# Kernel tuning notes

Hardware: AMD Instinct MI355X
Metric: run time of the kernel (lower is better)

The kernel has to match this reference:

```python
import jax, jax.numpy as jnp
import numpy as np

B, S, E, H, L, F = 64, 256, 480, 6, 8, 1920
D = E // H  # 80
VOCAB, MEL, CHORD = 4833, 257, 4833 - 257
EPS = 1e-5


def setup_inputs() -> dict:
    key = jax.random.key(0)
    ks = jax.random.split(key, 24)
    mel = jax.random.randint(ks[0], (B, S), 0, MEL)
    chd = MEL + jax.random.randint(ks[1], (B, S), 0, CHORD)
    pos = jnp.arange(S) % 2  # 0=melody, 1=chord
    input_tokens = jnp.where(pos[None, :] == 1, chd, mel)
    std = 0.02
    n = lambda k, shp: std * jax.random.normal(k, shp, dtype=jnp.float32)
    return {
        'input_tokens': input_tokens,
        'tok_emb': n(ks[2], (VOCAB, E)),
        'pos_emb': n(ks[3], (S, E)),
        'Wq': n(ks[4], (L, E, E)), 'bq': jnp.zeros((L, E)),
        'Wk': n(ks[5], (L, E, E)), 'bk': jnp.zeros((L, E)),
        'Wv': n(ks[6], (L, E, E)), 'bv': jnp.zeros((L, E)),
        'Wo': n(ks[7], (L, E, E)), 'bo': jnp.zeros((L, E)),
        'ln1_s': jnp.ones((L, E)), 'ln1_b': jnp.zeros((L, E)),
        'ln2_s': jnp.ones((L, E)), 'ln2_b': jnp.zeros((L, E)),
        'W1': n(ks[8], (L, F, E)), 'b1': jnp.zeros((L, F)),
        'W2': n(ks[9], (L, E, F)), 'b2': jnp.zeros((L, E)),
        'Wh': n(ks[10], (CHORD, E)), 'bh': jnp.zeros((CHORD,)),
    }


def _ln(x, s, b):
    mu = jnp.mean(x, -1, keepdims=True)
    var = jnp.var(x, -1, keepdims=True)
    return (x - mu) * jax.lax.rsqrt(var + EPS) * s + b


def reference(input_tokens, tok_emb, pos_emb, Wq, bq, Wk, bk, Wv, bv, Wo, bo,
              ln1_s, ln1_b, ln2_s, ln2_b, W1, b1, W2, b2, Wh, bh):
    x = tok_emb[input_tokens] + pos_emb[None, :, :]  # [B,S,E]
    causal = jnp.tril(jnp.ones((S, S), dtype=bool))  # True = keep
    scale = 1.0 / jnp.sqrt(jnp.float32(D))
    for i in range(L):
        h = _ln(x, ln1_s[i], ln1_b[i])
        q = (h @ Wq[i].T + bq[i]).reshape(B, S, H, D).transpose(0, 2, 1, 3)
        k = (h @ Wk[i].T + bk[i]).reshape(B, S, H, D).transpose(0, 2, 1, 3)
        v = (h @ Wv[i].T + bv[i]).reshape(B, S, H, D).transpose(0, 2, 1, 3)
        scores = jnp.einsum('bhsd,bhtd->bhst', q, k) * scale
        scores = jnp.where(causal[None, None], scores, -jnp.inf)
        attn = jax.nn.softmax(scores, axis=-1)
        o = jnp.einsum('bhst,bhtd->bhsd', attn, v)
        o = o.transpose(0, 2, 1, 3).reshape(B, S, E)
        x = x + (o @ Wo[i].T + bo[i])
        h2 = _ln(x, ln2_s[i], ln2_b[i])
        ff = jax.nn.gelu(h2 @ W1[i].T + b1[i], approximate=False) @ W2[i].T + b2[i]
        x = x + ff
    chord = x[:, 1::2, :]  # [B, S//2, E]
    return chord @ Wh.T + bh
```

## Files before the change

### kernel.cpp

```cpp
#include <hip/hip_runtime.h>
#include <hip/hip_bf16.h>
#include <math.h>

#define B_ 64
#define S_ 256
#define E_ 480
#define H_ 6
#define D_ 80
#define L_ 8
#define F_ 1920
#define CHORD_ 4576
#define TOKENS_ (B_*S_)
#define CROWS_ (B_*128)
#define QS_ 1440

typedef unsigned short u16;
typedef unsigned int u32;
typedef unsigned long long u64;
typedef __attribute__((ext_vector_type(8))) short short8;
typedef __attribute__((ext_vector_type(4))) float f32x4;
typedef __attribute__((ext_vector_type(4))) u32 u32x4;

__device__ __forceinline__ u16 f2bf(float f){
  u32 u = __float_as_uint(f);
// ... 53 lines not shown
  int i = blockIdx.x * 256 + threadIdx.x;
  if (i >= L_*QS_) return;
  int l = i / QS_, c = i - l*QS_;
  float v = (c < 480) ? bq[l*480 + c] : (c < 960) ? bk[l*480 + c - 480] : bv[l*480 + c - 960];
  dst[i] = v;
}

__global__ void embed_kernel(const int* __restrict__ tok,
                             const float* __restrict__ tok_emb,
                             const float* __restrict__ pos_emb,
                             float* __restrict__ x)
{
  int row = blockIdx.x;
  int s = row & (S_-1);
  int t = tok[row];
  const float* te = tok_emb + (size_t)t * E_;
  const float* pe = pos_emb + (size_t)s * E_;
  float* xr = x + (size_t)row * E_;
  for (int e = threadIdx.x; e < E_; e += blockDim.x)
    xr[e] = te[e] + pe[e];
}

__global__ __launch_bounds__(256) void ln_kernel(const float* __restrict__ x,
    const float* __restrict__ g, const float* __restrict__ b, u16* __restrict__ o)
{
  int wid = threadIdx.x >> 6, lane = threadIdx.x & 63;
  int row = blockIdx.x * 4 + wid;
  const float* xr = x + (size_t)row * E_;
  float v[8];
  #pragma unroll
  for (int i = 0; i < 7; ++i) v[i] = xr[lane + i*64];
  v[7] = (lane < 32) ? xr[448 + lane] : 0.f;
  float sum = 0.f, sq = 0.f;
  #pragma unroll
  for (int i = 0; i < 8; ++i){ sum += v[i]; sq += v[i]*v[i]; }
  #pragma unroll
  for (int m = 1; m < 64; m <<= 1){ sum += __shfl_xor(sum, m); sq += __shfl_xor(sq, m); }
  float mean = sum * (1.f/E_);
  float var  = sq  * (1.f/E_) - mean*mean;
  float rs = rsqrtf(var + 1e-5f);
  u16* orow = o + (size_t)row * E_;
  #pragma unroll
  for (int i = 0; i < 7; ++i){
    int idx = lane + i*64;
    orow[idx] = f2bf((v[i]-mean)*rs*g[idx] + b[idx]);
  }
  if (lane < 32){
    int idx = 448 + lane;
    orow[idx] = f2bf((v[7]-mean)*rs*g[idx] + b[idx]);
  }
}

template<int MODE>
__global__ __launch_bounds__(256, 4) void gemm_bf_kernel(const u16* __restrict__ A,
                            const u16* __restrict__ Wb, const float* __restrict__ bias,
                            u16* __restrict__ Cb, float* __restrict__ Cf,
                            int M, int N, int K, int ldc)
{
  __shared__ u16 As[2][128*32];
  __shared__ u16 Ws[2][128*32];
  const int tid = threadIdx.x;
  const int wid = tid >> 6, lane = tid & 63;
  const int wr = wid >> 1, wc = wid & 1;
  const int lr = lane & 15, kg = lane >> 4;
  const int kgs = kg ^ ((lr >> 1) & 3);
  int tx, ty;
  xcd_tile(gridDim.x, gridDim.y, tx, ty);
  const int m0 = ty * 128;
  const int n0 = tx * 128;

  const f32x4 zero = {0.f,0.f,0.f,0.f};
  f32x4 acc[4][4];
  #pragma unroll
  for (int i=0;i<4;i++)
    #pragma unroll
    for (int j=0;j<4;j++)
      acc[i][j] = zero;

  const int srow = tid >> 2;
  const int schunk = (tid & 3) ^ ((srow >> 1) & 3);
  const u16* ap0 = A + (size_t)(m0 + srow) * K + schunk*8;
  const u16* ap1 = ap0 + (size_t)64 * K;
  int r0 = n0 + srow, r1 = r0 + 64;
  if (r0 >= N) r0 = N-1;
  if (r1 >= N) r1 = N-1;
  const u16* wp0 = Wb + (size_t)r0 * K + schunk*8;
  const u16* wp1 = Wb + (size_t)r1 * K + schunk*8;

  #define STAGE(bb, k0) do { \
    char* ab = (char*)As[bb] + wid*1024; \
    char* wb_ = (char*)Ws[bb] + wid*1024; \
    async_cp16(ab,        ap0 + (k0)); \
    async_cp16(ab + 4096, ap1 + (k0)); \
    async_cp16(wb_,        wp0 + (k0)); \
    async_cp16(wb_ + 4096, wp1 + (k0)); \
  } while(0)

  const int nsteps = K >> 5;
  STAGE(0, 0);
  __syncthreads();
  int cur = 0;
  for (int ks = 0; ks < nsteps; ++ks){
    if (ks + 1 < nsteps) STAGE(cur^1, (ks+1) << 5);

    short8 af[4], wf[4];
    #pragma unroll
    for (int i=0;i<4;i++) af[i] = *(const short8*)&As[cur][(wr*64 + i*16 + lr)*32 + kgs*8];
    #pragma unroll
    for (int j=0;j<4;j++) wf[j] = *(const short8*)&Ws[cur][(wc*64 + j*16 + lr)*32 + kgs*8];
    #pragma unroll
    for (int i=0;i<4;i++)
      #pragma unroll
      for (int j=0;j<4;j++)
        acc[i][j] = __builtin_amdgcn_mfma_f32_16x16x32_bf16(af[i], wf[j], acc[i][j], 0, 0, 0);

    __syncthreads();
    cur ^= 1;
  }
  #undef STAGE

  #pragma unroll
  for (int i=0;i<4;i++){
    const int row = m0 + wr*64 + i*16 + kg*4;
    #pragma unroll
    for (int j=0;j<4;j++){
      const int col = n0 + wc*64 + j*16 + lr;
      if (col < N){
        const float bv = bias[col];
        #pragma unroll
        for (int q=0;q<4;q++){
          float val = acc[i][j][q] + bv;
          size_t off = (size_t)(row + q) * ldc + col;
          if (MODE == 0){
            Cb[off] = f2bf(val);
          } else if (MODE == 1){
            float gx = 0.5f * val * (1.f + erff(val * 0.70710678118654752f));
            Cb[off] = f2bf(gx);
          } else if (MODE == 2){
            Cf[off] += val;
          } else {
            Cf[off] = val;
          }
        }
      }
    }
  }
}

template<int MODE>
__global__ __launch_bounds__(256) void gemm_kernel(const u16* __restrict__ A, const float* __restrict__ W,
                            const float* __restrict__ bias,
                            u16* __restrict__ Cb, float* __restrict__ Cf,
                            int M, int N, int K, int ldc)
{
  __shared__ u16 As[128*32];
  __shared__ u16 Ws[128*32];
  const int tid = threadIdx.x;
  const int wid = tid >> 6, lane = tid & 63;
  const int wr = wid >> 1, wc = wid & 1;
  const int lr = lane & 15, kg = lane >> 4;
  int tx, ty;
  xcd_tile(gridDim.x, gridDim.y, tx, ty);
  const int m0 = ty * 128;
  const int n0 = tx * 128;

  const f32x4 zero = {0.f,0.f,0.f,0.f};
  f32x4 acc[4][4];
  #pragma unroll
  for (int i=0;i<4;i++)
    #pragma unroll
    for (int j=0;j<4;j++)
      acc[i][j] = zero;

  const int trow = tid >> 1;
  const int tcol = (tid & 1) * 16;
  const int wn = n0 + trow;
  const bool wok = wn < N;
  const float* wp = W + (size_t)wn * K + tcol;

  const u16* ap0 = A + (size_t)(m0 + (tid>>2)) * K + (tid&3)*8;
  const u16* ap1 = ap0 + (size_t)64 * K;
  char* lb0 = (char*)As + wid*1024;
  char* lb1 = (char*)As + 4096 + wid*1024;
  u32* wdst = (u32*)&Ws[trow*32 + tcol];

  const int nsteps = K >> 5;
  for (int ks = 0; ks < nsteps; ++ks){
    const int k0 = ks << 5;
    async_cp16(lb0, ap0 + k0);
    async_cp16(lb1, ap1 + k0);

    float wv[16];
    if (wok){
      const float4* s4 = (const float4*)(wp + k0);
      #pragma unroll
      for (int i=0;i<4;i++){
        float4 t4 = s4[i];
        wv[4*i]=t4.x; wv[4*i+1]=t4.y; wv[4*i+2]=t4.z; wv[4*i+3]=t4.w;
      }
    } else {
      #pragma unroll
      for (int i=0;i<16;i++) wv[i]=0.f;
    }
    u32 pk[8];
    #pragma unroll
    for (int i=0;i<8;i++) pk[i] = (u32)f2bf(wv[2*i]) | ((u32)f2bf(wv[2*i+1]) << 16);
    #pragma unroll
    for (int i=0;i<8;i++) wdst[i] = pk[i];

    __syncthreads();

    short8 af[4], wf[4];
    #pragma unroll
    for (int i=0;i<4;i++) af[i] = *(const short8*)&As[(wr*64 + i*16 + lr)*32 + kg*8];
    #pragma unroll
    for (int j=0;j<4;j++) wf[j] = *(const short8*)&Ws[(wc*64 + j*16 + lr)*32 + kg*8];
    #pragma unroll
    for (int i=0;i<4;i++)
      #pragma unroll
      for (int j=0;j<4;j++)
        acc[i][j] = __builtin_amdgcn_mfma_f32_16x16x32_bf16(af[i], wf[j], acc[i][j], 0, 0, 0);

    __syncthreads();
  }

  #pragma unroll
  for (int i=0;i<4;i++){
    const int row = m0 + wr*64 + i*16 + kg*4;
    #pragma unroll
    for (int j=0;j<4;j++){
      const int col = n0 + wc*64 + j*16 + lr;
      if (col < N){
        const float bv = bias[col];
        #pragma unroll
        for (int q=0;q<4;q++){
          float val = acc[i][j][q] + bv;
          size_t off = (size_t)(row + q) * ldc + col;
          if (MODE == 0){
            Cb[off] = f2bf(val);
          } else if (MODE == 1){
            float gx = 0.5f * val * (1.f + erff(val * 0.70710678118654752f));
            Cb[off] = f2bf(gx);
          } else if (MODE == 2){
            Cf[off] += val;
          } else {
            Cf[off] = val;
          }
        }
      }
    }
  }
}

#define KSTRIDE 104
#define VSTRIDE 264
__global__ __launch_bounds__(256) void attn_mfma_kernel(const u16* __restrict__ QKV,
                                                        u16* __restrict__ O)
{
  __shared__ u16 ks[256*KSTRIDE];
  __shared__ u16 vt[80*VSTRIDE];
  const int bh = blockIdx.x;
  const int b = bh / H_, h = bh - b*H_;
  const int tid = threadIdx.x;
  const int wv = tid >> 6, lane = tid & 63;
  const int q16 = lane & 15, g = lane >> 4;
  const size_t rowbase = (size_t)(b*S_ + tid) * QS_ + h * D_;

  {
    const uint4* kr = (const uint4*)(QKV + rowbase + 480);
    uint4 t0[10];
    #pragma unroll
    for (int i=0;i<10;i++) t0[i] = kr[i];
    u16* krow = &ks[tid*KSTRIDE];
    #pragma unroll
    for (int i=0;i<10;i++) *(uint4*)&krow[i*8] = t0[i];
    const uint4 z4 = {0,0,0,0};
    *(uint4*)&krow[80] = z4;
    *(uint4*)&krow[88] = z4;
  }
  {
    const u32* vr = (const u32*)(QKV + rowbase + 960);
    u32 t1[40];
    #pragma unroll
    for (int i=0;i<40;i++) t1[i] = vr[i];
    #pragma unroll
    for (int i=0;i<40;i++){
      vt[(2*i)*VSTRIDE + tid]   = (u16)(t1[i] & 0xffffu);
      vt[(2*i+1)*VSTRIDE + tid] = (u16)(t1[i] >> 16);
    }
  }
  short8 bq[4][3];
  const short8 z8 = {0,0,0,0,0,0,0,0};
  #pragma unroll
  for (int i=0;i<4;i++){
    const int qr = 16*wv + 64*i;
    const u16* qrow = QKV + (size_t)(b*S_ + qr + q16) * QS_ + h*D_;
    bq[i][0] = *(const short8*)&qrow[g*8];
    bq[i][1] = *(const short8*)&qrow[32 + g*8];
    bq[i][2] = (g < 2) ? *(const short8*)&qrow[64 + g*8] : z8;
  }
  __syncthreads();

  f32x4 o_[4][5];
  float m_[4], l_[4];
  #pragma unroll
  for (int i=0;i<4;i++){
    m_[i] = -1e30f; l_[i] = 0.f;
    #pragma unroll
    for (int j=0;j<5;j++) o_[i][j] = (f32x4){0.f,0.f,0.f,0.f};
  }
  const float scale = 0.1118033988749895f;
  const int ktmaxw = (16*wv + 207) >> 5;

  for (int kt = 0; kt <= ktmaxw; ++kt){
    short8 af[2][3];
    #pragma unroll
    for (int a=0;a<2;a++)
      #pragma unroll
      for (int kk=0;kk<3;kk++)
        af[a][kk] = *(const short8*)&ks[(32*kt + 16*a + q16)*KSTRIDE + kk*32 + g*8];
    short8 bvv[5];
    #pragma unroll
    for (int j=0;j<5;j++)
      bvv[j] = *(const short8*)&vt[(16*j + q16)*VSTRIDE + kt*32 + g*8];

    #pragma unroll
    for (int i=0;i<4;i++){
      const int qr = 16*wv + 64*i;
      if (kt > ((qr + 15) >> 5)) continue;
      f32x4 c0 = {0.f,0.f,0.f,0.f}, c1 = {0.f,0.f,0.f,0.f};
      #pragma unroll
      for (int kk=0;kk<3;kk++){
        c0 = __builtin_amdgcn_mfma_f32_16x16x32_bf16(af[0][kk], bq[i][kk], c0, 0, 0, 0);
        c1 = __builtin_amdgcn_mfma_f32_16x16x32_bf16(af[1][kk], bq[i][kk], c1, 0, 0, 0);
      }
      const int qglob = qr + q16;
      const int kb0 = 32*kt + 4*g;
      const bool diag = (32*kt + 31) > qr;
      float s0[4], s1[4];
      #pragma unroll
      for (int r=0;r<4;r++){
        s0[r] = c0[r] * scale;
        s1[r] = c1[r] * scale;
        if (diag){
          if (kb0 + r > qglob)      s0[r] = -3e38f;
          if (kb0 + 16 + r > qglob) s1[r] = -3e38f;
        }
      }
      float mx = fmaxf(fmaxf(fmaxf(s0[0],s0[1]),fmaxf(s0[2],s0[3])),
                       fmaxf(fmaxf(s1[0],s1[1]),fmaxf(s1[2],s1[3])));
      mx = fmaxf(mx, __shfl_xor(mx, 16));
      mx = fmaxf(mx, __shfl_xor(mx, 32));
      const float mnew = fmaxf(m_[i], mx);
      const float resc = __expf(m_[i] - mnew);
      float p0[4], p1[4], ps = 0.f;
      #pragma unroll
      for (int r=0;r<4;r++){
        p0[r] = __expf(s0[r] - mnew);
        p1[r] = __expf(s1[r] - mnew);
        ps += p0[r] + p1[r];
      }
      ps += __shfl_xor(ps, 16);
      ps += __shfl_xor(ps, 32);
      l_[i] = l_[i] * resc + ps;
      m_[i] = mnew;
      float fr[4];
      #pragma unroll
      for (int r=0;r<4;r++) fr[r] = __shfl(resc, 4*g + r);
      #pragma unroll
      for (int j=0;j<5;j++){
        #pragma unroll
        for (int r=0;r<4;r++) o_[i][j][r] *= fr[r];
      }
      u32 pw0 = (u32)f2bf(p0[0]) | ((u32)f2bf(p0[1]) << 16);
      u32 pw1 = (u32)f2bf(p0[2]) | ((u32)f2bf(p0[3]) << 16);
      u32 pw2 = (u32)f2bf(p1[0]) | ((u32)f2bf(p1[1]) << 16);
      u32 pw3 = (u32)f2bf(p1[2]) | ((u32)f2bf(p1[3]) << 16);
      const int s01 = ((((g<<1)&3)<<4) + q16) << 2;
      const int s23 = (((((g<<1)+1)&3)<<4) + q16) << 2;
      int rA0 = __builtin_amdgcn_ds_bpermute(s01, (int)pw0);
      int rB0 = __builtin_amdgcn_ds_bpermute(s01, (int)pw2);
      int rA1 = __builtin_amdgcn_ds_bpermute(s01, (int)pw1);
      int rB1 = __builtin_amdgcn_ds_bpermute(s01, (int)pw3);
      int rA2 = __builtin_amdgcn_ds_bpermute(s23, (int)pw0);
      int rB2 = __builtin_amdgcn_ds_bpermute(s23, (int)pw2);
      int rA3 = __builtin_amdgcn_ds_bpermute(s23, (int)pw1);
      int rB3 = __builtin_amdgcn_ds_bpermute(s23, (int)pw3);
      const bool lo = (g < 2);
      u32x4 rw = { (u32)(lo ? rA0 : rB0), (u32)(lo ? rA1 : rB1),
                   (u32)(lo ? rA2 : rB2), (u32)(lo ? rA3 : rB3) };
      short8 pa = __builtin_bit_cast(short8, rw);
      #pragma unroll
      for (int j=0;j<5;j++)
        o_[i][j] = __builtin_amdgcn_mfma_f32_16x16x32_bf16(pa, bvv[j], o_[i][j], 0, 0, 0);
    }
  }

  #pragma unroll
  for (int i=0;i<4;i++){
    const int qr = 16*wv + 64*i;
    const float inv = 1.f / l_[i];
    float fr[4];
    #pragma unroll
    for (int r=0;r<4;r++) fr[r] = __shfl(inv, 4*g + r);
    #pragma unroll
    for (int j=0;j<5;j++){
      #pragma unroll
      for (int r=0;r<4;r++){
        const int row = qr + 4*g + r;
        O[(size_t)(b*S_ + row) * E_ + h*D_ + 16*j + q16] = f2bf(o_[i][j][r] * fr[r]);
      }
    }
  }
}

__global__ void gather_kernel(const float* __restrict__ x, u16* __restrict__ cin)
{
  int i = blockIdx.x * 256 + threadIdx.x;
  if (i >= CROWS_*E_) return;
  int row = i / E_, col = i - row*E_;
  int b = row >> 7, r = row & 127;
  cin[i] = f2bf(x[((size_t)(b*S_ + 2*r + 1))*E_ + col]);
}

extern "C" void kernel_launch(void* const* d_in, const int* in_sizes, int n_in,
                              void* d_out, int out_size, void* d_ws, size_t ws_size,
                              hipStream_t stream)
{
  (void)in_sizes; (void)n_in; (void)out_size;
  const int*   tok     = (const int*)d_in[0];
  const float* tok_emb = (const float*)d_in[1];
  const float* pos_emb = (const float*)d_in[2];
  const float* Wq = (const float*)d_in[3];
  const float* bq = (const float*)d_in[4];
  const float* Wk = (const float*)d_in[5];
  const float* bk = (const float*)d_in[6];
  const float* Wv = (const float*)d_in[7];
  const float* bv = (const float*)d_in[8];
  const float* Wo = (const float*)d_in[9];
  const float* bo = (const float*)d_in[10];
  const float* ln1s = (const float*)d_in[11];
  const float* ln1b = (const float*)d_in[12];
  const float* ln2s = (const float*)d_in[13];
  const float* ln2b = (const float*)d_in[14];
  const float* W1 = (const float*)d_in[15];
  const float* b1 = (const float*)d_in[16];
  const float* W2 = (const float*)d_in[17];
  const float* b2 = (const float*)d_in[18];
  const float* Wh = (const float*)d_in[19];
  const float* bh = (const float*)d_in[20];

  char* p = (char*)d_ws;
  float* x  = (float*)p;            p += (size_t)TOKENS_*E_*4;
  u16* h    = (u16*)p;              p += (size_t)TOKENS_*E_*2;
  u16* qkv  = (u16*)p;
  u16* ao   = qkv + (size_t)TOKENS_*QS_;
  u16* ff1  = qkv;
  u16* cin  = h;
  p += (size_t)TOKENS_*QS_*2 + (size_t)TOKENS_*E_*2;

  const size_t szE  = (size_t)L_*E_*E_;
  const size_t szF  = (size_t)L_*F_*E_;
  const size_t szH  = (size_t)CHORD_*E_;
  u16* wqkv_bf = (u16*)p;            p += 3*szE*2;
  u16* wo_bf   = (u16*)p;            p += szE*2;
  u16* w1_bf   = (u16*)p;            p += szF*2;
  u16* w2_bf   = (u16*)p;            p += szF*2;
  u16* wh_bf   = (u16*)p;            p += szH*2;
  float* bqkv  = (float*)p;          p += (size_t)L_*QS_*4;
  const size_t need = (size_t)(p - (char*)d_ws);
  const bool bf16w = (ws_size >= need);

  embed_kernel<<<TOKENS_, 128, 0, stream>>>(tok, tok_emb, pos_emb, x);

  dim3 blk(256);
  dim3 gQKV(12, TOKENS_/128);
  dim3 gE(4, TOKENS_/128);
  dim3 gF1(15, TOKENS_/128);
  dim3 gHd(36, CROWS_/128);

  if (bf16w){
    qkv_cvt_kernel<<<2048, blk, 0, stream>>>(Wq, Wk, Wv, wqkv_bf);
    bias_cat_kernel<<<(L_*QS_ + 255)/256, blk, 0, stream>>>(bq, bk, bv, bqkv);
    cvt_kernel<<<1024, blk, 0, stream>>>(Wo, wo_bf, (int)(szE/4));
    cvt_kernel<<<1024, blk, 0, stream>>>(W1, w1_bf, (int)(szF/4));
    cvt_kernel<<<1024, blk, 0, stream>>>(W2, w2_bf, (int)(szF/4));
    cvt_kernel<<<1024, blk, 0, stream>>>(Wh, wh_bf, (int)(szH/4));
    for (int i = 0; i < L_; ++i){
      ln_kernel<<<TOKENS_/4, blk, 0, stream>>>(x, ln1s + i*E_, ln1b + i*E_, h);
      gemm_bf_kernel<0><<<gQKV, blk, 0, stream>>>(h, wqkv_bf + (size_t)i*3*E_*E_, bqkv + i*QS_, qkv, nullptr, TOKENS_, QS_, E_, QS_);
      attn_mfma_kernel<<<B_*H_, blk, 0, stream>>>(qkv, ao);
      gemm_bf_kernel<2><<<gE, blk, 0, stream>>>(ao, wo_bf + (size_t)i*E_*E_, bo + i*E_, nullptr, x, TOKENS_, E_, E_, E_);
      ln_kernel<<<TOKENS_/4, blk, 0, stream>>>(x, ln2s + i*E_, ln2b + i*E_, h);
      gemm_bf_kernel<1><<<gF1, blk, 0, stream>>>(h, w1_bf + (size_t)i*F_*E_, b1 + i*F_, ff1, nullptr, TOKENS_, F_, E_, F_);
      gemm_bf_kernel<2><<<gE, blk, 0, stream>>>(ff1, w2_bf + (size_t)i*E_*F_, b2 + i*E_, nullptr, x, TOKENS_, E_, F_, E_);
    }
    gather_kernel<<<(CROWS_*E_ + 255)/256, blk, 0, stream>>>(x, cin);
    gemm_bf_kernel<3><<<gHd, blk, 0, stream>>>(cin, wh_bf, bh, nullptr, (float*)d_out, CROWS_, CHORD_, E_, CHORD_);
  } else {
    for (int i = 0; i < L_; ++i){
      ln_kernel<<<TOKENS_/4, blk, 0, stream>>>(x, ln1s + i*E_, ln1b + i*E_, h);
      gemm_kernel<0><<<gE, blk, 0, stream>>>(h, Wq + (size_t)i*E_*E_, bq + i*E_, qkv, nullptr, TOKENS_, E_, E_, QS_);
      gemm_kernel<0><<<gE, blk, 0, stream>>>(h, Wk + (size_t)i*E_*E_, bk + i*E_, qkv + 480, nullptr, TOKENS_, E_, E_, QS_);
      gemm_kernel<0><<<gE, blk, 0, stream>>>(h, Wv + (size_t)i*E_*E_, bv + i*E_, qkv + 960, nullptr, TOKENS_, E_, E_, QS_);
      attn_mfma_kernel<<<B_*H_, blk, 0, stream>>>(qkv, ao);
      gemm_kernel<2><<<gE, blk, 0, stream>>>(ao, Wo + (size_t)i*E_*E_, bo + i*E_, nullptr, x, TOKENS_, E_, E_, E_);
      ln_kernel<<<TOKENS_/4, blk, 0, stream>>>(x, ln2s + i*E_, ln2b + i*E_, h);
      gemm_kernel<1><<<gF1, blk, 0, stream>>>(h, W1 + (size_t)i*F_*E_, b1 + i*F_, ff1, nullptr, TOKENS_, F_, E_, F_);
      gemm_kernel<2><<<gE, blk, 0, stream>>>(ff1, W2 + (size_t)i*E_*F_, b2 + i*E_, nullptr, x, TOKENS_, E_, F_, E_);
    }
    gather_kernel<<<(CROWS_*E_ + 255)/256, blk, 0, stream>>>(x, cin);
    gemm_kernel<3><<<gHd, blk, 0, stream>>>(cin, Wh, bh, nullptr, (float*)d_out, CROWS_, CHORD_, E_, CHORD_);
  }
}
```

Before: 2.124 ms.

## Enlarge bf16 GEMM block tile to 256x128 with 8x4 MFMA per wave

The bf16 GEMM kernel now computes a 256x128 output tile per block instead of 128x128. Each wave owns 128 rows and streams A fragments one at a time against four cached W fragments. The goal is more reuse of the weight tiles and fewer, larger blocks. This doubles the accumulator registers and the A shared memory, so launch bounds drop to 2 blocks per CU. Grids are halved in M, so small-N GEMMs such as N=480 launch only 256 blocks, which may underfill the GPU.

```diff
diff --git a/kernel.cpp b/kernel.cpp
--- a/kernel.cpp
+++ b/kernel.cpp
@@ -129,48 +129,52 @@
 }
 
 template<int MODE>
-__global__ __launch_bounds__(256, 4) void gemm_bf_kernel(const u16* __restrict__ A,
+__global__ __launch_bounds__(256, 2) void gemm_bf_kernel(const u16* __restrict__ A,
                             const u16* __restrict__ Wb, const float* __restrict__ bias,
                             u16* __restrict__ Cb, float* __restrict__ Cf,
                             int M, int N, int K, int ldc)
 {
-  __shared__ u16 As[2][128*32];
+  __shared__ u16 As[2][256*32];
   __shared__ u16 Ws[2][128*32];
   const int tid = threadIdx.x;
   const int wid = tid >> 6, lane = tid & 63;
-  const int wr = wid >> 1, wc = wid & 1;
+  const int wm = wid >> 1, wn = wid & 1;
   const int lr = lane & 15, kg = lane >> 4;
   const int kgs = kg ^ ((lr >> 1) & 3);
   int tx, ty;
   xcd_tile(gridDim.x, gridDim.y, tx, ty);
-  const int m0 = ty * 128;
+  const int m0 = ty * 256;
   const int n0 = tx * 128;
 
   const f32x4 zero = {0.f,0.f,0.f,0.f};
-  f32x4 acc[4][4];
-  #pragma unroll
-  for (int i=0;i<4;i++)
+  f32x4 acc[8][4];
+  #pragma unroll
+  for (int i=0;i<8;i++)
     #pragma unroll
     for (int j=0;j<4;j++)
       acc[i][j] = zero;
 
-  const int srow = tid >> 2;
-  const int schunk = (tid & 3) ^ ((srow >> 1) & 3);
-  const u16* ap0 = A + (size_t)(m0 + srow) * K + schunk*8;
-  const u16* ap1 = ap0 + (size_t)64 * K;
-  int r0 = n0 + srow, r1 = r0 + 64;
-  if (r0 >= N) r0 = N-1;
-  if (r1 >= N) r1 = N-1;
-  const u16* wp0 = Wb + (size_t)r0 * K + schunk*8;
-  const u16* wp1 = Wb + (size_t)r1 * K + schunk*8;
+  const int schunk = (lane & 3) ^ ((lane >> 3) & 3);
+  const int srow = wid*16 + (lane >> 2);
+  const u16* apA[4];
+  #pragma unroll
+  for (int it=0; it<4; ++it)
+    apA[it] = A + (size_t)(m0 + it*64 + srow) * K + schunk*8;
+  const u16* apW[2];
+  #pragma unroll
+  for (int it=0; it<2; ++it){
+    int r = n0 + it*64 + srow;
+    if (r >= N) r = N-1;
+    apW[it] = Wb + (size_t)r * K + schunk*8;
+  }
 
   #define STAGE(bb, k0) do { \
-    char* ab = (char*)As[bb] + wid*1024; \
-    char* wb_ = (char*)Ws[bb] + wid*1024; \
-    async_cp16(ab,        ap0 + (k0)); \
-    async_cp16(ab + 4096, ap1 + (k0)); \
-    async_cp16(wb_,        wp0 + (k0)); \
-    async_cp16(wb_ + 4096, wp1 + (k0)); \
+    _Pragma("unroll") \
+    for (int it=0; it<4; ++it) \
+      async_cp16((char*)As[bb] + (it*4 + wid)*1024, apA[it] + (k0)); \
+    _Pragma("unroll") \
+    for (int it=0; it<2; ++it) \
+      async_cp16((char*)Ws[bb] + (it*4 + wid)*1024, apW[it] + (k0)); \
   } while(0)
 
   const int nsteps = K >> 5;
@@ -180,16 +184,16 @@
   for (int ks = 0; ks < nsteps; ++ks){
     if (ks + 1 < nsteps) STAGE(cur^1, (ks+1) << 5);
 
-    short8 af[4], wf[4];
-    #pragma unroll
-    for (int i=0;i<4;i++) af[i] = *(const short8*)&As[cur][(wr*64 + i*16 + lr)*32 + kgs*8];
-    #pragma unroll
-    for (int j=0;j<4;j++) wf[j] = *(const short8*)&Ws[cur][(wc*64 + j*16 + lr)*32 + kgs*8];
-    #pragma unroll
-    for (int i=0;i<4;i++)
+    short8 wf[4];
+    #pragma unroll
+    for (int j=0;j<4;j++) wf[j] = *(const short8*)&Ws[cur][(wn*64 + j*16 + lr)*32 + kgs*8];
+    #pragma unroll
+    for (int i=0;i<8;i++){
+      short8 af = *(const short8*)&As[cur][(wm*128 + i*16 + lr)*32 + kgs*8];
       #pragma unroll
       for (int j=0;j<4;j++)
-        acc[i][j] = __builtin_amdgcn_mfma_f32_16x16x32_bf16(af[i], wf[j], acc[i][j], 0, 0, 0);
+        acc[i][j] = __builtin_amdgcn_mfma_f32_16x16x32_bf16(af, wf[j], acc[i][j], 0, 0, 0);
+    }
 
     __syncthreads();
     cur ^= 1;
@@ -197,11 +201,11 @@
   #undef STAGE
 
   #pragma unroll
-  for (int i=0;i<4;i++){
-    const int row = m0 + wr*64 + i*16 + kg*4;
+  for (int i=0;i<8;i++){
+    const int row = m0 + wm*128 + i*16 + kg*4;
     #pragma unroll
     for (int j=0;j<4;j++){
-      const int col = n0 + wc*64 + j*16 + lr;
+      const int col = n0 + wn*64 + j*16 + lr;
       if (col < N){
         const float bv = bias[col];
         #pragma unroll
@@ -551,10 +555,11 @@
   embed_kernel<<<TOKENS_, 128, 0, stream>>>(tok, tok_emb, pos_emb, x);
 
   dim3 blk(256);
-  dim3 gQKV(12, TOKENS_/128);
-  dim3 gE(4, TOKENS_/128);
-  dim3 gF1(15, TOKENS_/128);
-  dim3 gHd(36, CROWS_/128);
+  dim3 gQKV(12, TOKENS_/256);
+  dim3 gE(4, TOKENS_/256);
+  dim3 gF1(15, TOKENS_/256);
+  dim3 gW2(4, TOKENS_/256);
+  dim3 gHd(36, CROWS_/256);
 
   if (bf16w){
     qkv_cvt_kernel<<<2048, blk, 0, stream>>>(Wq, Wk, Wv, wqkv_bf);
@@ -570,23 +575,23 @@
       gemm_bf_kernel<2><<<gE, blk, 0, stream>>>(ao, wo_bf + (size_t)i*E_*E_, bo + i*E_, nullptr, x, TOKENS_, E_, E_, E_);
       ln_kernel<<<TOKENS_/4, blk, 0, stream>>>(x, ln2s + i*E_, ln2b + i*E_, h);
       gemm_bf_kernel<1><<<gF1, blk, 0, stream>>>(h, w1_bf + (size_t)i*F_*E_, b1 + i*F_, ff1, nullptr, TOKENS_, F_, E_, F_);
-      gemm_bf_kernel<2><<<gE, blk, 0, stream>>>(ff1, w2_bf + (size_t)i*E_*F_, b2 + i*E_, nullptr, x, TOKENS_, E_, F_, E_);
+      gemm_bf_kernel<2><<<gW2, blk, 0, stream>>>(ff1, w2_bf + (size_t)i*E_*F_, b2 + i*E_, nullptr, x, TOKENS_, E_, F_, E_);
     }
     gather_kernel<<<(CROWS_*E_ + 255)/256, blk, 0, stream>>>(x, cin);
     gemm_bf_kernel<3><<<gHd, blk, 0, stream>>>(cin, wh_bf, bh, nullptr, (float*)d_out, CROWS_, CHORD_, E_, CHORD_);
   } else {
     for (int i = 0; i < L_; ++i){
       ln_kernel<<<TOKENS_/4, blk, 0, stream>>>(x, ln1s + i*E_, ln1b + i*E_, h);
-      gemm_kernel<0><<<gE, blk, 0, stream>>>(h, Wq + (size_t)i*E_*E_, bq + i*E_, qkv, nullptr, TOKENS_, E_, E_, QS_);
-      gemm_kernel<0><<<gE, blk, 0, stream>>>(h, Wk + (size_t)i*E_*E_, bk + i*E_, qkv + 480, nullptr, TOKENS_, E_, E_, QS_);
-      gemm_kernel<0><<<gE, blk, 0, stream>>>(h, Wv + (size_t)i*E_*E_, bv + i*E_, qkv + 960, nullptr, TOKENS_, E_, E_, QS_);
+      gemm_kernel<0><<<dim3(4, 128), blk, 0, stream>>>(h, Wq + (size_t)i*E_*E_, bq + i*E_, qkv, nullptr, TOKENS_, E_, E_, QS_);
+      gemm_kernel<0><<<dim3(4, 128), blk, 0, stream>>>(h, Wk + (size_t)i*E_*E_, bk + i*E_, qkv + 480, nullptr, TOKENS_, E_, E_, QS_);
+      gemm_kernel<0><<<dim3(4, 128), blk, 0, stream>>>(h, Wv + (size_t)i*E_*E_, bv + i*E_, qkv + 960, nullptr, TOKENS_, E_, E_, QS_);
       attn_mfma_kernel<<<B_*H_, blk, 0, stream>>>(qkv, ao);
-      gemm_kernel<2><<<gE, blk, 0, stream>>>(ao, Wo + (size_t)i*E_*E_, bo + i*E_, nullptr, x, TOKENS_, E_, E_, E_);
+      gemm_kernel<2><<<dim3(4, 128), blk, 0, stream>>>(ao, Wo + (size_t)i*E_*E_, bo + i*E_, nullptr, x, TOKENS_, E_, E_, E_);
       ln_kernel<<<TOKENS_/4, blk, 0, stream>>>(x, ln2s + i*E_, ln2b + i*E_, h);
-      gemm_kernel<1><<<gF1, blk, 0, stream>>>(h, W1 + (size_t)i*F_*E_, b1 + i*F_, ff1, nullptr, TOKENS_, F_, E_, F_);
-      gemm_kernel<2><<<gE, blk, 0, stream>>>(ff1, W2 + (size_t)i*E_*F_, b2 + i*E_, nullptr, x, TOKENS_, E_, F_, E_);
+      gemm_kernel<1><<<dim3(15, 128), blk, 0, stream>>>(h, W1 + (size_t)i*F_*E_, b1 + i*F_, ff1, nullptr, TOKENS_, F_, E_, F_);
+      gemm_kernel<2><<<dim3(4, 128), blk, 0, stream>>>(ff1, W2 + (size_t)i*E_*F_, b2 + i*E_, nullptr, x, TOKENS_, E_, F_, E_);
     }
     gather_kernel<<<(CROWS_*E_ + 255)/256, blk, 0, stream>>>(x, cin);
-    gemm_kernel<3><<<gHd, blk, 0, stream>>>(cin, Wh, bh, nullptr, (float*)d_out, CROWS_, CHORD_, E_, CHORD_);
-  }
-}
+    gemm_kernel<3><<<dim3(36, 64), blk, 0, stream>>>(cin, Wh, bh, nullptr, (float*)d_out, CROWS_, CHORD_, E_, CHORD_);
+  }
+}
```

After: 2.736 ms. +28.8%, slower.

## Split-K the residual GEMMs with atomics and widen attention to 1024 threads

Applied to the files above, without the earlier changes.

The Wo and W2 residual GEMMs are split along K across blockIdx.z, into 2 and 4 slices. Each slice accumulates into the fp32 residual with atomicAdd, and only the first slice adds the bias. This gives more blocks for the narrow N=480 output, which before had only 4 column tiles, at the cost of atomic traffic and a summation order that is no longer fixed. The attention kernel now uses 16 waves per (batch, head), one 16-row query tile each, instead of 4 waves each looping over 4 tiles. K/V loading is split across the threads, which raises parallelism and lowers registers per thread but shrinks the causal loop per wave unevenly.

```diff
diff --git a/kernel.cpp b/kernel.cpp
--- a/kernel.cpp
+++ b/kernel.cpp
@@ -132,7 +132,7 @@
 __global__ __launch_bounds__(256, 4) void gemm_bf_kernel(const u16* __restrict__ A,
                             const u16* __restrict__ Wb, const float* __restrict__ bias,
                             u16* __restrict__ Cb, float* __restrict__ Cf,
-                            int M, int N, int K, int ldc)
+                            int M, int N, int K, int ldc, int CS)
 {
   __shared__ u16 As[2][128*32];
   __shared__ u16 Ws[2][128*32];
@@ -145,6 +145,8 @@
   xcd_tile(gridDim.x, gridDim.y, tx, ty);
   const int m0 = ty * 128;
   const int n0 = tx * 128;
+  const int kofs = blockIdx.z * CS;
+  int klen = K - kofs; if (klen > CS) klen = CS;
 
   const f32x4 zero = {0.f,0.f,0.f,0.f};
   f32x4 acc[4][4];
@@ -156,13 +158,13 @@
 
   const int srow = tid >> 2;
   const int schunk = (tid & 3) ^ ((srow >> 1) & 3);
-  const u16* ap0 = A + (size_t)(m0 + srow) * K + schunk*8;
+  const u16* ap0 = A + (size_t)(m0 + srow) * K + kofs + schunk*8;
   const u16* ap1 = ap0 + (size_t)64 * K;
   int r0 = n0 + srow, r1 = r0 + 64;
   if (r0 >= N) r0 = N-1;
   if (r1 >= N) r1 = N-1;
-  const u16* wp0 = Wb + (size_t)r0 * K + schunk*8;
-  const u16* wp1 = Wb + (size_t)r1 * K + schunk*8;
+  const u16* wp0 = Wb + (size_t)r0 * K + kofs + schunk*8;
+  const u16* wp1 = Wb + (size_t)r1 * K + kofs + schunk*8;
 
   #define STAGE(bb, k0) do { \
     char* ab = (char*)As[bb] + wid*1024; \
@@ -173,7 +175,7 @@
     async_cp16(wb_ + 4096, wp1 + (k0)); \
   } while(0)
 
-  const int nsteps = K >> 5;
+  const int nsteps = klen >> 5;
   STAGE(0, 0);
   __syncthreads();
   int cur = 0;
@@ -195,6 +197,113 @@
     cur ^= 1;
   }
   #undef STAGE
+
+  #pragma unroll
+  for (int i=0;i<4;i++){
+    const int row = m0 + wr*64 + i*16 + kg*4;
+    #pragma unroll
+    for (int j=0;j<4;j++){
+      const int col = n0 + wc*64 + j*16 + lr;
+      if (col < N){
+        const float bv = (MODE == 4) ? (kofs == 0 ? bias[col] : 0.f) : bias[col];
+        #pragma unroll
+        for (int q=0;q<4;q++){
+          float val = acc[i][j][q] + bv;
+          size_t off = (size_t)(row + q) * ldc + col;
+          if (MODE == 0){
+            Cb[off] = f2bf(val);
+          } else if (MODE == 1){
+            float gx = 0.5f * val * (1.f + erff(val * 0.70710678118654752f));
+            Cb[off] = f2bf(gx);
+          } else if (MODE == 2){
+            Cf[off] += val;
+          } else if (MODE == 4){
+            atomicAdd(&Cf[off], val);
+          } else {
+            Cf[off] = val;
+          }
+        }
+      }
+    }
+  }
+}
+
+template<int MODE>
+__global__ __launch_bounds__(256) void gemm_kernel(const u16* __restrict__ A, const float* __restrict__ W,
+                            const float* __restrict__ bias,
+                            u16* __restrict__ Cb, float* __restrict__ Cf,
+                            int M, int N, int K, int ldc)
+{
+  __shared__ u16 As[128*32];
+  __shared__ u16 Ws[128*32];
+  const int tid = threadIdx.x;
+  const int wid = tid >> 6, lane = tid & 63;
+  const int wr = wid >> 1, wc = wid & 1;
+  const int lr = lane & 15, kg = lane >> 4;
+  int tx, ty;
+  xcd_tile(gridDim.x, gridDim.y, tx, ty);
+  const int m0 = ty * 128;
+  const int n0 = tx * 128;
+
+  const f32x4 zero = {0.f,0.f,0.f,0.f};
+  f32x4 acc[4][4];
+  #pragma unroll
+  for (int i=0;i<4;i++)
+    #pragma unroll
+    for (int j=0;j<4;j++)
+      acc[i][j] = zero;
+
+  const int trow = tid >> 1;
+  const int tcol = (tid & 1) * 16;
+  const int wn = n0 + trow;
+  const bool wok = wn < N;
+  const float* wp = W + (size_t)wn * K + tcol;
+
+  const u16* ap0 = A + (size_t)(m0 + (tid>>2)) * K + (tid&3)*8;
+  const u16* ap1 = ap0 + (size_t)64 * K;
+  char* lb0 = (char*)As + wid*1024;
+  char* lb1 = (char*)As + 4096 + wid*1024;
+  u32* wdst = (u32*)&Ws[trow*32 + tcol];
+
+  const int nsteps = K >> 5;
+  for (int ks = 0; ks < nsteps; ++ks){
+    const int k0 = ks << 5;
+    async_cp16(lb0, ap0 + k0);
+    async_cp16(lb1, ap1 + k0);
+
+    float wv[16];
+    if (wok){
+      const float4* s4 = (const float4*)(wp + k0);
+      #pragma unroll
+      for (int i=0;i<4;i++){
+        float4 t4 = s4[i];
+        wv[4*i]=t4.x; wv[4*i+1]=t4.y; wv[4*i+2]=t4.z; wv[4*i+3]=t4.w;
+      }
+    } else {
+      #pragma unroll
+      for (int i=0;i<16;i++) wv[i]=0.f;
+    }
+    u32 pk[8];
+    #pragma unroll
+    for (int i=0;i<8;i++) pk[i] = (u32)f2bf(wv[2*i]) | ((u32)f2bf(wv[2*i+1]) << 16);
+    #pragma unroll
+    for (int i=0;i<8;i++) wdst[i] = pk[i];
+
+    __syncthreads();
+
+    short8 af[4], wf[4];
+    #pragma unroll
+    for (int i=0;i<4;i++) af[i] = *(const short8*)&As[(wr*64 + i*16 + lr)*32 + kg*8];
+    #pragma unroll
+    for (int j=0;j<4;j++) wf[j] = *(const short8*)&Ws[(wc*64 + j*16 + lr)*32 + kg*8];
+    #pragma unroll
+    for (int i=0;i<4;i++)
+      #pragma unroll
+      for (int j=0;j<4;j++)
+        acc[i][j] = __builtin_amdgcn_mfma_f32_16x16x32_bf16(af[i], wf[j], acc[i][j], 0, 0, 0);
+
+    __syncthreads();
+  }
 
   #pragma unroll
   for (int i=0;i<4;i++){
@@ -224,115 +333,10 @@
   }
 }
 
-template<int MODE>
-__global__ __launch_bounds__(256) void gemm_kernel(const u16* __restrict__ A, const float* __restrict__ W,
-                            const float* __restrict__ bias,
-                            u16* __restrict__ Cb, float* __restrict__ Cf,
-                            int M, int N, int K, int ldc)
-{
-  __shared__ u16 As[128*32];
-  __shared__ u16 Ws[128*32];
-  const int tid = threadIdx.x;
-  const int wid = tid >> 6, lane = tid & 63;
-  const int wr = wid >> 1, wc = wid & 1;
-  const int lr = lane & 15, kg = lane >> 4;
-  int tx, ty;
-  xcd_tile(gridDim.x, gridDim.y, tx, ty);
-  const int m0 = ty * 128;
-  const int n0 = tx * 128;
-
-  const f32x4 zero = {0.f,0.f,0.f,0.f};
-  f32x4 acc[4][4];
-  #pragma unroll
-  for (int i=0;i<4;i++)
-    #pragma unroll
-    for (int j=0;j<4;j++)
-      acc[i][j] = zero;
-
-  const int trow = tid >> 1;
-  const int tcol = (tid & 1) * 16;
-  const int wn = n0 + trow;
-  const bool wok = wn < N;
-  const float* wp = W + (size_t)wn * K + tcol;
-
-  const u16* ap0 = A + (size_t)(m0 + (tid>>2)) * K + (tid&3)*8;
-  const u16* ap1 = ap0 + (size_t)64 * K;
-  char* lb0 = (char*)As + wid*1024;
-  char* lb1 = (char*)As + 4096 + wid*1024;
-  u32* wdst = (u32*)&Ws[trow*32 + tcol];
-
-  const int nsteps = K >> 5;
-  for (int ks = 0; ks < nsteps; ++ks){
-    const int k0 = ks << 5;
-    async_cp16(lb0, ap0 + k0);
-    async_cp16(lb1, ap1 + k0);
-
-    float wv[16];
-    if (wok){
-      const float4* s4 = (const float4*)(wp + k0);
-      #pragma unroll
-      for (int i=0;i<4;i++){
-        float4 t4 = s4[i];
-        wv[4*i]=t4.x; wv[4*i+1]=t4.y; wv[4*i+2]=t4.z; wv[4*i+3]=t4.w;
-      }
-    } else {
-      #pragma unroll
-      for (int i=0;i<16;i++) wv[i]=0.f;
-    }
-    u32 pk[8];
-    #pragma unroll
-    for (int i=0;i<8;i++) pk[i] = (u32)f2bf(wv[2*i]) | ((u32)f2bf(wv[2*i+1]) << 16);
-    #pragma unroll
-    for (int i=0;i<8;i++) wdst[i] = pk[i];
-
-    __syncthreads();
-
-    short8 af[4], wf[4];
-    #pragma unroll
-    for (int i=0;i<4;i++) af[i] = *(const short8*)&As[(wr*64 + i*16 + lr)*32 + kg*8];
-    #pragma unroll
-    for (int j=0;j<4;j++) wf[j] = *(const short8*)&Ws[(wc*64 + j*16 + lr)*32 + kg*8];
-    #pragma unroll
-    for (int i=0;i<4;i++)
-      #pragma unroll
-      for (int j=0;j<4;j++)
-        acc[i][j] = __builtin_amdgcn_mfma_f32_16x16x32_bf16(af[i], wf[j], acc[i][j], 0, 0, 0);
-
-    __syncthreads();
-  }
-
-  #pragma unroll
-  for (int i=0;i<4;i++){
-    const int row = m0 + wr*64 + i*16 + kg*4;
-    #pragma unroll
-    for (int j=0;j<4;j++){
-      const int col = n0 + wc*64 + j*16 + lr;
-      if (col < N){
-        const float bv = bias[col];
-        #pragma unroll
-        for (int q=0;q<4;q++){
-          float val = acc[i][j][q] + bv;
-          size_t off = (size_t)(row + q) * ldc + col;
-          if (MODE == 0){
-            Cb[off] = f2bf(val);
-          } else if (MODE == 1){
-            float gx = 0.5f * val * (1.f + erff(val * 0.70710678118654752f));
-            Cb[off] = f2bf(gx);
-          } else if (MODE == 2){
-            Cf[off] += val;
-          } else {
-            Cf[off] = val;
-          }
-        }
-      }
-    }
-  }
-}
-
 #define KSTRIDE 104
 #define VSTRIDE 264
-__global__ __launch_bounds__(256) void attn_mfma_kernel(const u16* __restrict__ QKV,
-                                                        u16* __restrict__ O)
+__global__ __launch_bounds__(1024) void attn_mfma_kernel(const u16* __restrict__ QKV,
+                                                         u16* __restrict__ O)
 {
   __shared__ u16 ks[256*KSTRIDE];
   __shared__ u16 vt[80*VSTRIDE];
@@ -341,55 +345,54 @@
   const int tid = threadIdx.x;
   const int wv = tid >> 6, lane = tid & 63;
   const int q16 = lane & 15, g = lane >> 4;
-  const size_t rowbase = (size_t)(b*S_ + tid) * QS_ + h * D_;
-
+
+  if (tid < 512){
+    const int row = tid >> 1, half = tid & 1;
+    const uint4* kr = (const uint4*)(QKV + (size_t)(b*S_ + row) * QS_ + h*D_ + 480);
+    uint4 t0[5];
+    #pragma unroll
+    for (int i=0;i<5;i++) t0[i] = kr[half*5 + i];
+    u16* krow = &ks[row*KSTRIDE];
+    #pragma unroll
+    for (int i=0;i<5;i++) *(uint4*)&krow[(half*5 + i)*8] = t0[i];
+    if (half){
+      const uint4 z4 = {0,0,0,0};
+      *(uint4*)&krow[80] = z4;
+      *(uint4*)&krow[88] = z4;
+    }
+  } else {
+    const int t = tid - 512, row = t >> 1, half = t & 1;
+    const u32* vr = (const u32*)(QKV + (size_t)(b*S_ + row) * QS_ + h*D_ + 960);
+    u32 t1[20];
+    #pragma unroll
+    for (int i=0;i<20;i++) t1[i] = vr[half*20 + i];
+    #pragma unroll
+    for (int i=0;i<20;i++){
+      const int d = 2*(half*20 + i);
+      vt[d*VSTRIDE + row]     = (u16)(t1[i] & 0xffffu);
+      vt[(d+1)*VSTRIDE + row] = (u16)(t1[i] >> 16);
+    }
+  }
+  const int qr = 16*wv;
+  short8 bq0, bq1, bq2;
   {
-    const uint4* kr = (const uint4*)(QKV + rowbase + 480);
-    uint4 t0[10];
-    #pragma unroll
-    for (int i=0;i<10;i++) t0[i] = kr[i];
-    u16* krow = &ks[tid*KSTRIDE];
-    #pragma unroll
-    for (int i=0;i<10;i++) *(uint4*)&krow[i*8] = t0[i];
-    const uint4 z4 = {0,0,0,0};
-    *(uint4*)&krow[80] = z4;
-    *(uint4*)&krow[88] = z4;
-  }
-  {
-    const u32* vr = (const u32*)(QKV + rowbase + 960);
-    u32 t1[40];
-    #pragma unroll
-    for (int i=0;i<40;i++) t1[i] = vr[i];
-    #pragma unroll
-    for (int i=0;i<40;i++){
-      vt[(2*i)*VSTRIDE + tid]   = (u16)(t1[i] & 0xffffu);
-      vt[(2*i+1)*VSTRIDE + tid] = (u16)(t1[i] >> 16);
-    }
-  }
-  short8 bq[4][3];
-  const short8 z8 = {0,0,0,0,0,0,0,0};
-  #pragma unroll
-  for (int i=0;i<4;i++){
-    const int qr = 16*wv + 64*i;
+    const short8 z8 = {0,0,0,0,0,0,0,0};
     const u16* qrow = QKV + (size_t)(b*S_ + qr + q16) * QS_ + h*D_;
-    bq[i][0] = *(const short8*)&qrow[g*8];
-    bq[i][1] = *(const short8*)&qrow[32 + g*8];
-    bq[i][2] = (g < 2) ? *(const short8*)&qrow[64 + g*8] : z8;
+    bq0 = *(const short8*)&qrow[g*8];
+    bq1 = *(const short8*)&qrow[32 + g*8];
+    bq2 = (g < 2) ? *(const short8*)&qrow[64 + g*8] : z8;
   }
   __syncthreads();
 
-  f32x4 o_[4][5];
-  float m_[4], l_[4];
-  #pragma unroll
-  for (int i=0;i<4;i++){
-    m_[i] = -1e30f; l_[i] = 0.f;
-    #pragma unroll
-    for (int j=0;j<5;j++) o_[i][j] = (f32x4){0.f,0.f,0.f,0.f};
-  }
+  f32x4 o_[5];
+  #pragma unroll
+  for (int j=0;j<5;j++) o_[j] = (f32x4){0.f,0.f,0.f,0.f};
+  float m_ = -1e30f, l_ = 0.f;
   const float scale = 0.1118033988749895f;
-  const int ktmaxw = (16*wv + 207) >> 5;
-
-  for (int kt = 0; kt <= ktmaxw; ++kt){
+  const int qglob = qr + q16;
+  const int ktmax = (qr + 15) >> 5;
+
+  for (int kt = 0; kt <= ktmax; ++kt){
     short8 af[2][3];
     #pragma unroll
     for (int a=0;a<2;a++)
@@ -401,92 +404,84 @@
     for (int j=0;j<5;j++)
       bvv[j] = *(const short8*)&vt[(16*j + q16)*VSTRIDE + kt*32 + g*8];
 
-    #pragma unroll
-    for (int i=0;i<4;i++){
-      const int qr = 16*wv + 64*i;
-      if (kt > ((qr + 15) >> 5)) continue;
-      f32x4 c0 = {0.f,0.f,0.f,0.f}, c1 = {0.f,0.f,0.f,0.f};
-      #pragma unroll
-      for (int kk=0;kk<3;kk++){
-        c0 = __builtin_amdgcn_mfma_f32_16x16x32_bf16(af[0][kk], bq[i][kk], c0, 0, 0, 0);
-        c1 = __builtin_amdgcn_mfma_f32_16x16x32_bf16(af[1][kk], bq[i][kk], c1, 0, 0, 0);
+    f32x4 c0 = {0.f,0.f,0.f,0.f}, c1 = {0.f,0.f,0.f,0.f};
+    c0 = __builtin_amdgcn_mfma_f32_16x16x32_bf16(af[0][0], bq0, c0, 0, 0, 0);
+    c1 = __builtin_amdgcn_mfma_f32_16x16x32_bf16(af[1][0], bq0, c1, 0, 0, 0);
+    c0 = __builtin_amdgcn_mfma_f32_16x16x32_bf16(af[0][1], bq1, c0, 0, 0, 0);
+    c1 = __builtin_amdgcn_mfma_f32_16x16x32_bf16(af[1][1], bq1, c1, 0, 0, 0);
+    c0 = __builtin_amdgcn_mfma_f32_16x16x32_bf16(af[0][2], bq2, c0, 0, 0, 0);
+    c1 = __builtin_amdgcn_mfma_f32_16x16x32_bf16(af[1][2], bq2, c1, 0, 0, 0);
+
+    const int kb0 = 32*kt + 4*g;
+    const bool diag = (32*kt + 31) > qr;
+    float s0[4], s1[4];
+    #pragma unroll
+    for (int r=0;r<4;r++){
+      s0[r] = c0[r] * scale;
+      s1[r] = c1[r] * scale;
+      if (diag){
+        if (kb0 + r > qglob)      s0[r] = -3e38f;
+        if (kb0 + 16 + r > qglob) s1[r] = -3e38f;
       }
-      const int qglob = qr + q16;
-      const int kb0 = 32*kt + 4*g;
-      const bool diag = (32*kt + 31) > qr;
-      float s0[4], s1[4];
-      #pragma unroll
-      for (int r=0;r<4;r++){
-        s0[r] = c0[r] * scale;
-        s1[r] = c1[r] * scale;
-        if (diag){
-          if (kb0 + r > qglob)      s0[r] = -3e38f;
-          if (kb0 + 16 + r > qglob) s1[r] = -3e38f;
-        }
-      }
-      float mx = fmaxf(fmaxf(fmaxf(s0[0],s0[1]),fmaxf(s0[2],s0[3])),
-                       fmaxf(fmaxf(s1[0],s1[1]),fmaxf(s1[2],s1[3])));
-      mx = fmaxf(mx, __shfl_xor(mx, 16));
-      mx = fmaxf(mx, __shfl_xor(mx, 32));
-      const float mnew = fmaxf(m_[i], mx);
-      const float resc = __expf(m_[i] - mnew);
-      float p0[4], p1[4], ps = 0.f;
-      #pragma unroll
-      for (int r=0;r<4;r++){
-        p0[r] = __expf(s0[r] - mnew);
-        p1[r] = __expf(s1[r] - mnew);
-        ps += p0[r] + p1[r];
-      }
-      ps += __shfl_xor(ps, 16);
-      ps += __shfl_xor(ps, 32);
-      l_[i] = l_[i] * resc + ps;
-      m_[i] = mnew;
-      float fr[4];
-      #pragma unroll
-      for (int r=0;r<4;r++) fr[r] = __shfl(resc, 4*g + r);
-      #pragma unroll
-      for (int j=0;j<5;j++){
-        #pragma unroll
-        for (int r=0;r<4;r++) o_[i][j][r] *= fr[r];
-      }
-      u32 pw0 = (u32)f2bf(p0[0]) | ((u32)f2bf(p0[1]) << 16);
-      u32 pw1 = (u32)f2bf(p0[2]) | ((u32)f2bf(p0[3]) << 16);
-      u32 pw2 = (u32)f2bf(p1[0]) | ((u32)f2bf(p1[1]) << 16);
-      u32 pw3 = (u32)f2bf(p1[2]) | ((u32)f2bf(p1[3]) << 16);
-      const int s01 = ((((g<<1)&3)<<4) + q16) << 2;
-      const int s23 = (((((g<<1)+1)&3)<<4) + q16) << 2;
-      int rA0 = __builtin_amdgcn_ds_bpermute(s01, (int)pw0);
-      int rB0 = __builtin_amdgcn_ds_bpermute(s01, (int)pw2);
-      int rA1 = __builtin_amdgcn_ds_bpermute(s01, (int)pw1);
-      int rB1 = __builtin_amdgcn_ds_bpermute(s01, (int)pw3);
-      int rA2 = __builtin_amdgcn_ds_bpermute(s23, (int)pw0);
-      int rB2 = __builtin_amdgcn_ds_bpermute(s23, (int)pw2);
-      int rA3 = __builtin_amdgcn_ds_bpermute(s23, (int)pw1);
-      int rB3 = __builtin_amdgcn_ds_bpermute(s23, (int)pw3);
-      const bool lo = (g < 2);
-      u32x4 rw = { (u32)(lo ? rA0 : rB0), (u32)(lo ? rA1 : rB1),
-                   (u32)(lo ? rA2 : rB2), (u32)(lo ? rA3 : rB3) };
-      short8 pa = __builtin_bit_cast(short8, rw);
-      #pragma unroll
-      for (int j=0;j<5;j++)
-        o_[i][j] = __builtin_amdgcn_mfma_f32_16x16x32_bf16(pa, bvv[j], o_[i][j], 0, 0, 0);
-    }
-  }
-
-  #pragma unroll
-  for (int i=0;i<4;i++){
-    const int qr = 16*wv + 64*i;
-    const float inv = 1.f / l_[i];
+    }
+    float mx = fmaxf(fmaxf(fmaxf(s0[0],s0[1]),fmaxf(s0[2],s0[3])),
+                     fmaxf(fmaxf(s1[0],s1[1]),fmaxf(s1[2],s1[3])));
+    mx = fmaxf(mx, __shfl_xor(mx, 16));
+    mx = fmaxf(mx, __shfl_xor(mx, 32));
+    const float mnew = fmaxf(m_, mx);
+    const float resc = __expf(m_ - mnew);
+    float p0[4], p1[4], ps = 0.f;
+    #pragma unroll
+    for (int r=0;r<4;r++){
+      p0[r] = __expf(s0[r] - mnew);
+      p1[r] = __expf(s1[r] - mnew);
+      ps += p0[r] + p1[r];
+    }
+    ps += __shfl_xor(ps, 16);
+    ps += __shfl_xor(ps, 32);
+    l_ = l_ * resc + ps;
+    m_ = mnew;
     float fr[4];
     #pragma unroll
-    for (int r=0;r<4;r++) fr[r] = __shfl(inv, 4*g + r);
+    for (int r=0;r<4;r++) fr[r] = __shfl(resc, 4*g + r);
     #pragma unroll
     for (int j=0;j<5;j++){
       #pragma unroll
-      for (int r=0;r<4;r++){
-        const int row = qr + 4*g + r;
-        O[(size_t)(b*S_ + row) * E_ + h*D_ + 16*j + q16] = f2bf(o_[i][j][r] * fr[r]);
-      }
+      for (int r=0;r<4;r++) o_[j][r] *= fr[r];
+    }
+    u32 pw0 = (u32)f2bf(p0[0]) | ((u32)f2bf(p0[1]) << 16);
+    u32 pw1 = (u32)f2bf(p0[2]) | ((u32)f2bf(p0[3]) << 16);
+    u32 pw2 = (u32)f2bf(p1[0]) | ((u32)f2bf(p1[1]) << 16);
+    u32 pw3 = (u32)f2bf(p1[2]) | ((u32)f2bf(p1[3]) << 16);
+    const int s01 = ((((g<<1)&3)<<4) + q16) << 2;
+    const int s23 = (((((g<<1)+1)&3)<<4) + q16) << 2;
+    int rA0 = __builtin_amdgcn_ds_bpermute(s01, (int)pw0);
+    int rB0 = __builtin_amdgcn_ds_bpermute(s01, (int)pw2);
+    int rA1 = __builtin_amdgcn_ds_bpermute(s01, (int)pw1);
+    int rB1 = __builtin_amdgcn_ds_bpermute(s01, (int)pw3);
+    int rA2 = __builtin_amdgcn_ds_bpermute(s23, (int)pw0);
+    int rB2 = __builtin_amdgcn_ds_bpermute(s23, (int)pw2);
+    int rA3 = __builtin_amdgcn_ds_bpermute(s23, (int)pw1);
+    int rB3 = __builtin_amdgcn_ds_bpermute(s23, (int)pw3);
+    const bool lo = (g < 2);
+    u32x4 rw = { (u32)(lo ? rA0 : rB0), (u32)(lo ? rA1 : rB1),
+                 (u32)(lo ? rA2 : rB2), (u32)(lo ? rA3 : rB3) };
+    short8 pa = __builtin_bit_cast(short8, rw);
+    #pragma unroll
+    for (int j=0;j<5;j++)
+      o_[j] = __builtin_amdgcn_mfma_f32_16x16x32_bf16(pa, bvv[j], o_[j], 0, 0, 0);
+  }
+
+  const float inv = 1.f / l_;
+  float fr[4];
+  #pragma unroll
+  for (int r=0;r<4;r++) fr[r] = __shfl(inv, 4*g + r);
+  #pragma unroll
+  for (int j=0;j<5;j++){
+    #pragma unroll
+    for (int r=0;r<4;r++){
+      const int row = qr + 4*g + r;
+      O[(size_t)(b*S_ + row) * E_ + h*D_ + 16*j + q16] = f2bf(o_[j][r] * fr[r]);
     }
   }
 }
@@ -552,8 +547,9 @@
 
   dim3 blk(256);
   dim3 gQKV(12, TOKENS_/128);
-  dim3 gE(4, TOKENS_/128);
+  dim3 gWo(4, TOKENS_/128, 2);
   dim3 gF1(15, TOKENS_/128);
+  dim3 gW2(4, TOKENS_/128, 4);
   dim3 gHd(36, CROWS_/128);
 
   if (bf16w){
@@ -565,28 +561,28 @@
     cvt_kernel<<<1024, blk, 0, stream>>>(Wh, wh_bf, (int)(szH/4));
     for (int i = 0; i < L_; ++i){
       ln_kernel<<<TOKENS_/4, blk, 0, stream>>>(x, ln1s + i*E_, ln1b + i*E_, h);
-      gemm_bf_kernel<0><<<gQKV, blk, 0, stream>>>(h, wqkv_bf + (size_t)i*3*E_*E_, bqkv + i*QS_, qkv, nullptr, TOKENS_, QS_, E_, QS_);
-      attn_mfma_kernel<<<B_*H_, blk, 0, stream>>>(qkv, ao);
-      gemm_bf_kernel<2><<<gE, blk, 0, stream>>>(ao, wo_bf + (size_t)i*E_*E_, bo + i*E_, nullptr, x, TOKENS_, E_, E_, E_);
+      gemm_bf_kernel<0><<<gQKV, blk, 0, stream>>>(h, wqkv_bf + (size_t)i*3*E_*E_, bqkv + i*QS_, qkv, nullptr, TOKENS_, QS_, E_, QS_, E_);
+      attn_mfma_kernel<<<B_*H_, dim3(1024), 0, stream>>>(qkv, ao);
+      gemm_bf_kernel<4><<<gWo, blk, 0, stream>>>(ao, wo_bf + (size_t)i*E_*E_, bo + i*E_, nullptr, x, TOKENS_, E_, E_, E_, 256);
       ln_kernel<<<TOKENS_/4, blk, 0, stream>>>(x, ln2s + i*E_, ln2b + i*E_, h);
-      gemm_bf_kernel<1><<<gF1, blk, 0, stream>>>(h, w1_bf + (size_t)i*F_*E_, b1 + i*F_, ff1, nullptr, TOKENS_, F_, E_, F_);
-      gemm_bf_kernel<2><<<gE, blk, 0, stream>>>(ff1, w2_bf + (size_t)i*E_*F_, b2 + i*E_, nullptr, x, TOKENS_, E_, F_, E_);
+      gemm_bf_kernel<1><<<gF1, blk, 0, stream>>>(h, w1_bf + (size_t)i*F_*E_, b1 + i*F_, ff1, nullptr, TOKENS_, F_, E_, F_, E_);
+      gemm_bf_kernel<4><<<gW2, blk, 0, stream>>>(ff1, w2_bf + (size_t)i*E_*F_, b2 + i*E_, nullptr, x, TOKENS_, E_, F_, E_, 480);
     }
     gather_kernel<<<(CROWS_*E_ + 255)/256, blk, 0, stream>>>(x, cin);
-    gemm_bf_kernel<3><<<gHd, blk, 0, stream>>>(cin, wh_bf, bh, nullptr, (float*)d_out, CROWS_, CHORD_, E_, CHORD_);
+    gemm_bf_kernel<3><<<gHd, blk, 0, stream>>>(cin, wh_bf, bh, nullptr, (float*)d_out, CROWS_, CHORD_, E_, CHORD_, E_);
   } else {
     for (int i = 0; i < L_; ++i){
       ln_kernel<<<TOKENS_/4, blk, 0, stream>>>(x, ln1s + i*E_, ln1b + i*E_, h);
-      gemm_kernel<0><<<gE, blk, 0, stream>>>(h, Wq + (size_t)i*E_*E_, bq + i*E_, qkv, nullptr, TOKENS_, E_, E_, QS_);
-      gemm_kernel<0><<<gE, blk, 0, stream>>>(h, Wk + (size_t)i*E_*E_, bk + i*E_, qkv + 480, nullptr, TOKENS_, E_, E_, QS_);
-      gemm_kernel<0><<<gE, blk, 0, stream>>>(h, Wv + (size_t)i*E_*E_, bv + i*E_, qkv + 960, nullptr, TOKENS_, E_, E_, QS_);
-      attn_mfma_kernel<<<B_*H_, blk, 0, stream>>>(qkv, ao);
-      gemm_kernel<2><<<gE, blk, 0, stream>>>(ao, Wo + (size_t)i*E_*E_, bo + i*E_, nullptr, x, TOKENS_, E_, E_, E_);
+      gemm_kernel<0><<<dim3(4, 128), blk, 0, stream>>>(h, Wq + (size_t)i*E_*E_, bq + i*E_, qkv, nullptr, TOKENS_, E_, E_, QS_);
+      gemm_kernel<0><<<dim3(4, 128), blk, 0, stream>>>(h, Wk + (size_t)i*E_*E_, bk + i*E_, qkv + 480, nullptr, TOKENS_, E_, E_, QS_);
+      gemm_kernel<0><<<dim3(4, 128), blk, 0, stream>>>(h, Wv + (size_t)i*E_*E_, bv + i*E_, qkv + 960, nullptr, TOKENS_, E_, E_, QS_);
+      attn_mfma_kernel<<<B_*H_, dim3(1024), 0, stream>>>(qkv, ao);
+      gemm_kernel<2><<<dim3(4, 128), blk, 0, stream>>>(ao, Wo + (size_t)i*E_*E_, bo + i*E_, nullptr, x, TOKENS_, E_, E_, E_);
       ln_kernel<<<TOKENS_/4, blk, 0, stream>>>(x, ln2s + i*E_, ln2b + i*E_, h);
-      gemm_kernel<1><<<gF1, blk, 0, stream>>>(h, W1 + (size_t)i*F_*E_, b1 + i*F_, ff1, nullptr, TOKENS_, F_, E_, F_);
-      gemm_kernel<2><<<gE, blk, 0, stream>>>(ff1, W2 + (size_t)i*E_*F_, b2 + i*E_, nullptr, x, TOKENS_, E_, F_, E_);
+      gemm_kernel<1><<<dim3(15, 128), blk, 0, stream>>>(h, W1 + (size_t)i*F_*E_, b1 + i*F_, ff1, nullptr, TOKENS_, F_, E_, F_);
+      gemm_kernel<2><<<dim3(4, 128), blk, 0, stream>>>(ff1, W2 + (size_t)i*E_*F_, b2 + i*E_, nullptr, x, TOKENS_, E_, F_, E_);
     }
     gather_kernel<<<(CROWS_*E_ + 255)/256, blk, 0, stream>>>(x, cin);
-    gemm_kernel<3><<<gHd, blk, 0, stream>>>(cin, Wh, bh, nullptr, (float*)d_out, CROWS_, CHORD_, E_, CHORD_);
-  }
-}
+    gemm_kernel<3><<<dim3(36, 64), blk, 0, stream>>>(cin, Wh, bh, nullptr, (float*)d_out, CROWS_, CHORD_, E_, CHORD_);
+  }
+}
```

Measured after the change: 2.680 ms. 26.1% more time.
